# Performance work log

Measured on AMD Instinct MI355X. Metric: run time of the kernel, lower is better.

Reference implementation:

```python
import jax, jax.numpy as jnp
import numpy as np

B, C, M, H, K, V = 2, 2048, 1024, 16, 64, 64


def setup_inputs() -> dict:
    key = jax.random.key(0)
    ks = jax.random.split(key, 6)
    mscale = 1.0 / np.sqrt(M)
    vscale = 1.0 / np.sqrt(V)
    return {
        "kvinput": jax.random.normal(ks[0], (B, C, M), dtype=jnp.float32),
        "qinput": jax.random.normal(ks[1], (B, C, M), dtype=jnp.float32),
        "wq": jax.random.normal(ks[2], (H, M, K), dtype=jnp.float32) * mscale,
        "wk": jax.random.normal(ks[3], (H, M, K), dtype=jnp.float32) * mscale,
        "wv": jax.random.normal(ks[4], (H, M, V), dtype=jnp.float32) * mscale,
        "wo": jax.random.normal(ks[5], (H, V, M), dtype=jnp.float32) * vscale,
    }


def reference(kvinput, qinput, wq, wk, wv, wo):
    scale = 1.0 / np.sqrt(K).astype(np.float32)
    kval = jnp.einsum('bcm,hmk->bhck', kvinput, wk)
    qval = jnp.einsum('bcm,hmk->bhck', qinput, wq)
    vval = jnp.einsum('bcm,hmv->bhcv', kvinput, wv)
    # NOTE: c indexes keys, d indexes queries (faithful to the original einsum order)
    alogit = jnp.einsum('bhck,bhdk->bhcd', kval, qval)
    # additive -100 mask on strictly-lower triangle (key pos c > query pos d), as in source
    mask = jnp.tri(alogit.shape[2], k=-1, dtype=alogit.dtype) * -100.0
    alogit = alogit + mask
    att = jax.nn.softmax(alogit * scale, axis=2)  # softmax over key axis c
    pre = jnp.einsum('bhcd,bhcv->bhdv', att, vval)
    out = jnp.einsum('bhcv,hvm->bcm', pre, wo)
    return out
```

## Files before the change

### kernel.cpp

```cpp
#include <hip/hip_runtime.h>
#include <hip/hip_bf16.h>

typedef __bf16 bf16;
typedef __attribute__((ext_vector_type(8))) __bf16 bf16x8;
typedef __attribute__((ext_vector_type(4))) __bf16 bf16x4;
typedef __attribute__((ext_vector_type(4))) float f32x4;

#define NB 2
#define NC 2048
#define NM 1024
#define NH 16
#define NK 64
#define NV 64
#define NHV 1024

#define MFMA(a, b, c) __builtin_amdgcn_mfma_f32_16x16x32_bf16((a), (b), (c), 0, 0, 0)

__global__ __launch_bounds__(256) void prep_kernel(
    const float* __restrict__ qin, const float* __restrict__ kvin,
    const float* __restrict__ wq, const float* __restrict__ wk,
    const float* __restrict__ wv, const float* __restrict__ wo,
    bf16* __restrict__ qb, bf16* __restrict__ kvb,
    bf16* __restrict__ wqT, bf16* __restrict__ wkT,
    bf16* __restrict__ wvT, bf16* __restrict__ woT) {
  __shared__ float tile[32][33];
  const int bx = blockIdx.x;
  const int tid = threadIdx.x;
  if (bx < 1024) {
    const float4* src = (const float4*)((bx < 512) ? qin : kvin);
    bf16x4* dst = (bf16x4*)((bx < 512) ? qb : kvb);
    int base = (bx & 511) * 2048;
#pragma unroll
    for (int k = 0; k < 8; ++k) {
      int i = base + k * 256 + tid;
      float4 v = src[i];
      bf16x4 o;
      o.x = (bf16)v.x; o.y = (bf16)v.y; o.z = (bf16)v.z; o.w = (bf16)v.w;
      dst[i] = o;
    }
  } else if (bx < 4096) {
    const int sel = (bx >> 10) - 1;
    const float* w = (sel == 0) ? wq : (sel == 1) ? wk : wv;
    bf16* wT = (sel == 0) ? wqT : (sel == 1) ? wkT : wvT;
    const int t = bx & 1023;
    const int k0 = (t & 1) * 32, m0 = ((t >> 1) & 31) * 32, h = t >> 6;
    const int tx = tid & 31, ty = tid >> 5;
#pragma unroll
    for (int dy = 0; dy < 32; dy += 8)
      tile[ty + dy][tx] = w[((size_t)h * NM + m0 + ty + dy) * NK + k0 + tx];
    __syncthreads();
#pragma unroll
    for (int dy = 0; dy < 32; dy += 8)
      wT[((size_t)h * NK + k0 + ty + dy) * NM + m0 + tx] = (bf16)tile[tx][ty + dy];
  } else {
    const int t = bx & 1023;
    const int hv0 = (t & 31) * 32, m0 = (t >> 5) * 32;
    const int tx = tid & 31, ty = tid >> 5;
#pragma unroll
    for (int dy = 0; dy < 32; dy += 8)
      tile[ty + dy][tx] = wo[((size_t)(hv0 + ty + dy)) * NM + m0 + tx];
    __syncthreads();
#pragma unroll
    for (int dy = 0; dy < 32; dy += 8)
      woT[((size_t)(m0 + ty + dy)) * NHV + hv0 + tx] = (bf16)tile[tx][ty + dy];
  }
}


#define GEMM_BODY(Aptr, BTptr)                                                     \
  __shared__ bf16 Al[128 * 64], Bl[128 * 64];                                      \
  const int m0 = blockIdx.x * 128, n0 = blockIdx.y * 128;                          \
  const int tid = threadIdx.x;                                                     \
  const int w = tid >> 6, lane = tid & 63, lr = lane & 15, lg = lane >> 4;         \
  const int wm = w >> 1, wn = w & 1;                                               \
  f32x4 acc[4][4] = {};                                                            \
  for (int k0 = 0; k0 < 1024; k0 += 64) {                                          \
    _Pragma("unroll")                                                              \
    for (int it = 0; it < 4; ++it) {                                               \
      int id = it * 256 + tid;                                                     \
      int row = id >> 3, ch = (id & 7) ^ (row & 7);                                \
      __builtin_amdgcn_global_load_lds(                                            \
          (const __attribute__((address_space(1))) void*)(Aptr +                   \
              (size_t)(m0 + row) * 1024 + k0 + ch * 8),                            \
          (__attribute__((address_space(3))) void*)&Al[(it * 256 + w * 64) * 8],   \
          16, 0, 0);                                                               \
      __builtin_amdgcn_global_load_lds(                                            \
          (const __attribute__((address_space(1))) void*)(BTptr +                  \
              (size_t)(n0 + row) * 1024 + k0 + ch * 8),                            \
          (__attribute__((address_space(3))) void*)&Bl[(it * 256 + w * 64) * 8],   \
          16, 0, 0);                                                               \
    }                                                                              \
    __syncthreads();                                                               \
    _Pragma("unroll")                                                              \
    for (int ks = 0; ks < 2; ++ks) {                                               \
      bf16x8 a[4], bb[4];                                                          \
      _Pragma("unroll")                                                            \
      for (int i = 0; i < 4; ++i) {                                                \
        int ra = wm * 64 + i * 16 + lr;                                            \
        a[i] = *reinterpret_cast<const bf16x8*>(                                   \
            &Al[ra * 64 + (((ks * 4 + lg) ^ (ra & 7)) << 3)]);                     \
        int rb = wn * 64 + i * 16 + lr;                                            \
        bb[i] = *reinterpret_cast<const bf16x8*>(                                  \
            &Bl[rb * 64 + (((ks * 4 + lg) ^ (rb & 7)) << 3)]);                     \
      }                                                                            \
      _Pragma("unroll")                                                            \
      for (int mi = 0; mi < 4; ++mi)                                               \
        _Pragma("unroll")                                                          \
        for (int ni = 0; ni < 4; ++ni)                                             \
          acc[mi][ni] = MFMA(a[mi], bb[ni], acc[mi][ni]);                          \
    }                                                                              \
    __syncthreads();                                                               \
  }

__global__ __launch_bounds__(256) void proj_fused_kernel(
    const bf16* __restrict__ qb, const bf16* __restrict__ kvb,
    const bf16* __restrict__ wqT, const bf16* __restrict__ wkT,
    const bf16* __restrict__ wvT, bf16* __restrict__ Qp,
    bf16* __restrict__ Kp, bf16* __restrict__ VpT) {
  const int z = blockIdx.z;
  const bf16* Ain = (z == 0) ? qb : kvb;
  const bf16* BTin = (z == 0) ? wqT : (z == 1) ? wkT : wvT;
  GEMM_BODY(Ain, BTin)
  if (z < 2) {
    bf16* dst = (z == 0) ? Qp : Kp;
#pragma unroll
    for (int mi = 0; mi < 4; ++mi)
#pragma unroll
      for (int ni = 0; ni < 4; ++ni)
#pragma unroll
        for (int j = 0; j < 4; ++j) {
          int gm = m0 + wm * 64 + mi * 16 + 4 * lg + j;
          int gn = n0 + wn * 64 + ni * 16 + lr;
          dst[(((size_t)((gm >> 11) * 16 + (gn >> 6)) * 2048 + (gm & 2047)) << 6) +
              (gn & 63)] = (bf16)acc[mi][ni][j];
        }
  } else {
#pragma unroll
    for (int mi = 0; mi < 4; ++mi)
#pragma unroll
      for (int ni = 0; ni < 4; ++ni) {
        int gm0 = m0 + wm * 64 + mi * 16 + 4 * lg;
        int gn = n0 + wn * 64 + ni * 16 + lr;
        bf16x4 pv;
#pragma unroll
        for (int j = 0; j < 4; ++j) pv[j] = (bf16)acc[mi][ni][j];
        *reinterpret_cast<bf16x4*>(
            &VpT[((size_t)((gm0 >> 11) * 16 + (gn >> 6)) * 64 + (gn & 63)) * 2048 +
                 (gm0 & 2047)]) = pv;
      }
  }
}

__global__ __launch_bounds__(256) void out_gemm_kernel(
    const bf16* __restrict__ preb, const bf16* __restrict__ woT,
    float* __restrict__ out) {
  __shared__ bf16 Al[64 * 64], Bl[128 * 64];
  const int m0 = blockIdx.x * 64, n0 = blockIdx.y * 128;
  const int tid = threadIdx.x;
  const int w = tid >> 6, lane = tid & 63, lr = lane & 15, lg = lane >> 4;
  const int wm = w >> 1, wn = w & 1;
  f32x4 acc[2][4] = {};
  for (int k0 = 0; k0 < 1024; k0 += 64) {
#pragma unroll
    for (int it = 0; it < 2; ++it) {
      int id = it * 256 + tid;
      int row = id >> 3, ch = (id & 7) ^ (row & 7);
      __builtin_amdgcn_global_load_lds(
          (const __attribute__((address_space(1))) void*)(preb +
              (size_t)(m0 + row) * 1024 + k0 + ch * 8),
          (__attribute__((address_space(3))) void*)&Al[(it * 256 + w * 64) * 8],
          16, 0, 0);
    }
#pragma unroll
    for (int it = 0; it < 4; ++it) {
      int id = it * 256 + tid;
      int row = id >> 3, ch = (id & 7) ^ (row & 7);
      __builtin_amdgcn_global_load_lds(
          (const __attribute__((address_space(1))) void*)(woT +
              (size_t)(n0 + row) * 1024 + k0 + ch * 8),
          (__attribute__((address_space(3))) void*)&Bl[(it * 256 + w * 64) * 8],
          16, 0, 0);
    }
    __syncthreads();
#pragma unroll
    for (int ks = 0; ks < 2; ++ks) {
      bf16x8 a[2], bb[4];
#pragma unroll
      for (int i = 0; i < 2; ++i) {
        int ra = wm * 32 + i * 16 + lr;
        a[i] = *reinterpret_cast<const bf16x8*>(
            &Al[ra * 64 + (((ks * 4 + lg) ^ (ra & 7)) << 3)]);
      }
#pragma unroll
      for (int i = 0; i < 4; ++i) {
        int rb = wn * 64 + i * 16 + lr;
        bb[i] = *reinterpret_cast<const bf16x8*>(
            &Bl[rb * 64 + (((ks * 4 + lg) ^ (rb & 7)) << 3)]);
      }
#pragma unroll
      for (int mi = 0; mi < 2; ++mi)
#pragma unroll
        for (int ni = 0; ni < 4; ++ni)
          acc[mi][ni] = MFMA(a[mi], bb[ni], acc[mi][ni]);
    }
    __syncthreads();
  }
#pragma unroll
  for (int mi = 0; mi < 2; ++mi)
#pragma unroll
    for (int ni = 0; ni < 4; ++ni)
#pragma unroll
      for (int j = 0; j < 4; ++j) {
        int gm = m0 + wm * 32 + mi * 16 + 4 * lg + j;
        int gn = n0 + wn * 64 + ni * 16 + lr;
        out[(size_t)gm * 1024 + gn] = acc[mi][ni][j];
      }
}

__global__ __launch_bounds__(256) void attn_kernel(
    const bf16* __restrict__ Qp, const bf16* __restrict__ Kp,
    const bf16* __restrict__ VpT, bf16* __restrict__ preb) {
  __shared__ bf16 Klds[2][64 * 64];
  __shared__ bf16 Vlds[2][64 * 64];
  __shared__ bf16 Plds[4][16 * 64];

  const int bh = blockIdx.y;
  const int b = bh >> 4, h = bh & 15;
  const int j = (blockIdx.x + blockIdx.y) & 31;
  const int tid = threadIdx.x;
  const int w = tid >> 6;
  const int lane = tid & 63;
  const int lr = lane & 15, lg = lane >> 4;
  const int qb0 = j * 64 + w * 16;

  const bf16* Qb = Qp + (size_t)bh * NC * NK;
  const bf16* Kb = Kp + (size_t)bh * NC * NK;
  const bf16* Vb = VpT + (size_t)bh * NV * NC;
  char* PL = (char*)&Plds[w][0];

  bf16x8 qfr[2];
#pragma unroll
  for (int s = 0; s < 2; ++s)
    qfr[s] = *reinterpret_cast<const bf16x8*>(
        Qb + (size_t)(qb0 + lr) * NK + s * 32 + lg * 8);

  f32x4 acc[4] = {};
  float llane = 0.f;

  const float SC = 0.18033688f;
  const float O_IN = -11.541560f;
  const float O_MK = -29.575249f;

  const int srow = tid >> 3;
  const int sch0 = tid & 7;
  const int ch0 = sch0 ^ (srow & 7), ch1 = sch0 ^ ((32 + srow) & 7);
  const bf16* k0p = Kb + (size_t)srow * NK + ch0 * 8;
  const bf16* k1p = Kb + (size_t)(32 + srow) * NK + ch1 * 8;
  const bf16* v0p = Vb + (size_t)srow * NC + ch0 * 8;
  const bf16* v1p = Vb + (size_t)(32 + srow) * NC + ch1 * 8;

  auto STAGE = [&](int buf) {
    __builtin_amdgcn_global_load_lds(
        (const __attribute__((address_space(1))) void*)k0p,
        (__attribute__((address_space(3))) void*)&Klds[buf][(w * 8) * 64], 16, 0, 0);
    __builtin_amdgcn_global_load_lds(
        (const __attribute__((address_space(1))) void*)k1p,
        (__attribute__((address_space(3))) void*)&Klds[buf][(32 + w * 8) * 64], 16, 0, 0);
    __builtin_amdgcn_global_load_lds(
        (const __attribute__((address_space(1))) void*)v0p,
        (__attribute__((address_space(3))) void*)&Vlds[buf][(w * 8) * 64], 16, 0, 0);
    __builtin_amdgcn_global_load_lds(
        (const __attribute__((address_space(1))) void*)v1p,
        (__attribute__((address_space(3))) void*)&Vlds[buf][(32 + w * 8) * 64], 16, 0, 0);
    k0p += 64 * NK; k1p += 64 * NK; v0p += 64; v1p += 64;
  };

  const int nt = (j == 0) ? (NC / 64) : (j + 1);

  STAGE(0);
  asm volatile("s_waitcnt vmcnt(0)" ::: "memory");
  __syncthreads();

  for (int t = 0; t < nt; ++t) {
    const int cur = t & 1;
    const int c0 = t * 64;
    if (t + 1 < nt) STAGE(cur ^ 1);

    const char* KL = (const char*)&Klds[cur][0];
    const char* VL = (const char*)&Vlds[cur][0];

    f32x4 S[4] = {};
    __builtin_amdgcn_s_setprio(1);
#pragma unroll
    for (int s = 0; s < 2; ++s)
#pragma unroll
      for (int kf = 0; kf < 4; ++kf) {
        bf16x8 kfr = *reinterpret_cast<const bf16x8*>(
            KL + (kf * 16 + lr) * 128 + (((s * 4 + lg) ^ (lr & 7)) << 4));
        S[kf] = MFMA(kfr, qfr[s], S[kf]);
      }
    __builtin_amdgcn_s_setprio(0);

    {
      bf16x4 pq[4];
      float lp[4];
      if (t < j) {
#pragma unroll
        for (int kf = 0; kf < 4; ++kf) {
          float s0 = exp2f(fmaf(S[kf][0], SC, O_IN));
          float s1 = exp2f(fmaf(S[kf][1], SC, O_IN));
          float s2 = exp2f(fmaf(S[kf][2], SC, O_IN));
          float s3 = exp2f(fmaf(S[kf][3], SC, O_IN));
          pq[kf][0] = (bf16)s0; pq[kf][1] = (bf16)s1;
          pq[kf][2] = (bf16)s2; pq[kf][3] = (bf16)s3;
          lp[kf] = (s0 + s1) + (s2 + s3);
        }
      } else if (t == j) {
        const int qg = qb0 + lr;
#pragma unroll
        for (int kf = 0; kf < 4; ++kf) {
          float sv[4];
#pragma unroll
          for (int i = 0; i < 4; ++i) {
            int key = c0 + kf * 16 + 4 * lg + i;
            sv[i] = exp2f(fmaf(S[kf][i], SC, (key > qg) ? O_MK : O_IN));
            pq[kf][i] = (bf16)sv[i];
          }
          lp[kf] = (sv[0] + sv[1]) + (sv[2] + sv[3]);
        }
      } else {
#pragma unroll
        for (int kf = 0; kf < 4; ++kf) {
          float sv[4];
#pragma unroll
          for (int i = 0; i < 4; ++i) {
            sv[i] = exp2f(fmaf(S[kf][i], SC, O_MK));
            pq[kf][i] = (bf16)sv[i];
          }
          lp[kf] = (sv[0] + sv[1]) + (sv[2] + sv[3]);
        }
      }
      llane += (lp[0] + lp[1]) + (lp[2] + lp[3]);
#pragma unroll
      for (int kf = 0; kf < 4; ++kf) {
        int cc = 2 * kf + (lg >> 1);
        *reinterpret_cast<bf16x4*>(
            PL + lr * 128 + ((cc ^ (lr & 7)) << 4) + (lg & 1) * 8) = pq[kf];
      }
    }

    __builtin_amdgcn_s_setprio(1);
#pragma unroll
    for (int s2 = 0; s2 < 2; ++s2) {
      bf16x8 pa = *reinterpret_cast<const bf16x8*>(
          PL + lr * 128 + (((s2 * 4 + lg) ^ (lr & 7)) << 4));
#pragma unroll
      for (int vf = 0; vf < 4; ++vf) {
        bf16x8 vfr = *reinterpret_cast<const bf16x8*>(
            VL + (vf * 16 + lr) * 128 + (((s2 * 4 + lg) ^ (lr & 7)) << 4));
        acc[vf] = MFMA(pa, vfr, acc[vf]);
      }
    }
    __builtin_amdgcn_s_setprio(0);

    asm volatile("s_waitcnt vmcnt(0)" ::: "memory");
    __syncthreads();
  }

  llane += __shfl_xor(llane, 16);
  llane += __shfl_xor(llane, 32);
  float li[4];
#pragma unroll
  for (int i = 0; i < 4; ++i) li[i] = 1.0f / __shfl(llane, 4 * lg + i);
  bf16* ob = preb + ((size_t)b * NC) * NHV + (size_t)h * NV;
#pragma unroll
  for (int vf = 0; vf < 4; ++vf)
#pragma unroll
    for (int i = 0; i < 4; ++i) {
      int d = qb0 + 4 * lg + i;
      ob[(size_t)d * NHV + vf * 16 + lr] = (bf16)(acc[vf][i] * li[i]);
    }
}


extern "C" void kernel_launch(void* const* d_in, const int* in_sizes, int n_in,
                              void* d_out, int out_size, void* d_ws, size_t ws_size,
                              hipStream_t stream) {
  const float* kvinput = (const float*)d_in[0];
  const float* qinput  = (const float*)d_in[1];
  const float* wq = (const float*)d_in[2];
  const float* wk = (const float*)d_in[3];
  const float* wv = (const float*)d_in[4];
  const float* wo = (const float*)d_in[5];
  float* out = (float*)d_out;

  char* ws = (char*)d_ws;
  bf16* qb   = (bf16*)(ws + 0);
  bf16* kvb  = (bf16*)(ws + 8388608);
  bf16* wqT  = (bf16*)(ws + 16777216);
  bf16* wkT  = (bf16*)(ws + 18874368);
  bf16* wvT  = (bf16*)(ws + 20971520);
  bf16* woT  = (bf16*)(ws + 23068672);
  bf16* Qp   = (bf16*)(ws + 25165824);
  bf16* Kp   = (bf16*)(ws + 33554432);
  bf16* VpT  = (bf16*)(ws + 41943040);
  bf16* preb = (bf16*)(ws + 50331648);

  prep_kernel<<<5120, 256, 0, stream>>>(qinput, kvinput, wq, wk, wv, wo,
                                        qb, kvb, wqT, wkT, wvT, woT);

  dim3 pg(32, 8, 3);
  proj_fused_kernel<<<pg, 256, 0, stream>>>(qb, kvb, wqT, wkT, wvT, Qp, Kp, VpT);

  dim3 ag(32, NB * NH);
  attn_kernel<<<ag, 256, 0, stream>>>(Qp, Kp, VpT, preb);

  dim3 og(64, 8);
  out_gemm_kernel<<<og, 256, 0, stream>>>(preb, woT, out);
}
```

Baseline: 126.5 us.

## Remap attention query-block order via lookup table and drop s_setprio hints

Replaces the rotating (blockIdx.x+blockIdx.y)&31 query-block assignment with a per-head-group lookup table. Work per block varies a lot with causal length (block 0 does the full sequence), so the table orders blocks so that heavy and light ones are spread differently across CUs. The staging pointers are now computed from the tile index instead of being incremented, and the s_setprio wave-priority hints around the MFMA sections are removed. This trades a small table load and extra address arithmetic for a possibly better load balance. Dropping the priority hints may change how waves interleave.

```diff
diff --git a/kernel.cpp b/kernel.cpp
--- a/kernel.cpp
+++ b/kernel.cpp
@@ -15,6 +15,13 @@
 #define NHV 1024
 
 #define MFMA(a, b, c) __builtin_amdgcn_mfma_f32_16x16x32_bf16((a), (b), (c), 0, 0, 0)
+
+__device__ const unsigned char JTAB[4][32] = {
+  {0,11,12,13, 1,2,3,4,5,6,7,8,9,10, 14,15,16,17,18,19,20,21,22,23,24,25,26,27,28,29,30,31},
+  {11,0,13,12, 31,30,29,28,27,26,25,24,23,22, 21,20,19,18,17,16,15,14, 10,9,8,7,6,5,4,3,2,1},
+  {12,13,0,11, 18,19,20,21,22,23,24,25,26,27,28,29,30,31, 1,2,3,4,5,6,7,8,9,10, 14,15,16,17},
+  {13,12,11,0, 17,16,15,14, 10,9,8,7,6,5,4,3,2,1, 31,30,29,28,27,26,25,24,23,22,21,20,19,18},
+};
 
 __global__ __launch_bounds__(256) void prep_kernel(
     const float* __restrict__ qin, const float* __restrict__ kvin,
@@ -226,7 +233,7 @@
 
   const int bh = blockIdx.y;
   const int b = bh >> 4, h = bh & 15;
-  const int j = (blockIdx.x + blockIdx.y) & 31;
+  const int j = JTAB[blockIdx.y >> 3][blockIdx.x];
   const int tid = threadIdx.x;
   const int w = tid >> 6;
   const int lane = tid & 63;
@@ -253,44 +260,39 @@
 
   const int srow = tid >> 3;
   const int sch0 = tid & 7;
-  const int ch0 = sch0 ^ (srow & 7), ch1 = sch0 ^ ((32 + srow) & 7);
-  const bf16* k0p = Kb + (size_t)srow * NK + ch0 * 8;
-  const bf16* k1p = Kb + (size_t)(32 + srow) * NK + ch1 * 8;
-  const bf16* v0p = Vb + (size_t)srow * NC + ch0 * 8;
-  const bf16* v1p = Vb + (size_t)(32 + srow) * NC + ch1 * 8;
-
-  auto STAGE = [&](int buf) {
-    __builtin_amdgcn_global_load_lds(
-        (const __attribute__((address_space(1))) void*)k0p,
-        (__attribute__((address_space(3))) void*)&Klds[buf][(w * 8) * 64], 16, 0, 0);
-    __builtin_amdgcn_global_load_lds(
-        (const __attribute__((address_space(1))) void*)k1p,
-        (__attribute__((address_space(3))) void*)&Klds[buf][(32 + w * 8) * 64], 16, 0, 0);
-    __builtin_amdgcn_global_load_lds(
-        (const __attribute__((address_space(1))) void*)v0p,
-        (__attribute__((address_space(3))) void*)&Vlds[buf][(w * 8) * 64], 16, 0, 0);
-    __builtin_amdgcn_global_load_lds(
-        (const __attribute__((address_space(1))) void*)v1p,
-        (__attribute__((address_space(3))) void*)&Vlds[buf][(32 + w * 8) * 64], 16, 0, 0);
-    k0p += 64 * NK; k1p += 64 * NK; v0p += 64; v1p += 64;
+  auto STAGE = [&](int buf, int c0) {
+#pragma unroll
+    for (int i = 0; i < 2; ++i) {
+      int row = i * 32 + srow;
+      int ch = sch0 ^ (row & 7);
+      __builtin_amdgcn_global_load_lds(
+          (const __attribute__((address_space(1))) void*)(
+              Kb + (size_t)(c0 + row) * NK + ch * 8),
+          (__attribute__((address_space(3))) void*)&Klds[buf][(i * 32 + w * 8) * 64],
+          16, 0, 0);
+      __builtin_amdgcn_global_load_lds(
+          (const __attribute__((address_space(1))) void*)(
+              Vb + (size_t)row * NC + c0 + ch * 8),
+          (__attribute__((address_space(3))) void*)&Vlds[buf][(i * 32 + w * 8) * 64],
+          16, 0, 0);
+    }
   };
 
   const int nt = (j == 0) ? (NC / 64) : (j + 1);
 
-  STAGE(0);
+  STAGE(0, 0);
   asm volatile("s_waitcnt vmcnt(0)" ::: "memory");
   __syncthreads();
 
   for (int t = 0; t < nt; ++t) {
     const int cur = t & 1;
     const int c0 = t * 64;
-    if (t + 1 < nt) STAGE(cur ^ 1);
+    if (t + 1 < nt) STAGE(cur ^ 1, (t + 1) * 64);
 
     const char* KL = (const char*)&Klds[cur][0];
     const char* VL = (const char*)&Vlds[cur][0];
 
     f32x4 S[4] = {};
-    __builtin_amdgcn_s_setprio(1);
 #pragma unroll
     for (int s = 0; s < 2; ++s)
 #pragma unroll
@@ -299,7 +301,6 @@
             KL + (kf * 16 + lr) * 128 + (((s * 4 + lg) ^ (lr & 7)) << 4));
         S[kf] = MFMA(kfr, qfr[s], S[kf]);
       }
-    __builtin_amdgcn_s_setprio(0);
 
     {
       bf16x4 pq[4];
@@ -349,7 +350,6 @@
       }
     }
 
-    __builtin_amdgcn_s_setprio(1);
 #pragma unroll
     for (int s2 = 0; s2 < 2; ++s2) {
       bf16x8 pa = *reinterpret_cast<const bf16x8*>(
@@ -361,7 +361,6 @@
         acc[vf] = MFMA(pa, vfr, acc[vf]);
       }
     }
-    __builtin_amdgcn_s_setprio(0);
 
     asm volatile("s_waitcnt vmcnt(0)" ::: "memory");
     __syncthreads();
```

After: 123.5 us. 2.4% less time.
